# Optimization experiments

Measured on AMD Instinct MI355X. Metric: run time of the kernel, lower is better.

## Reference

```python
import jax, jax.numpy as jnp
import numpy as np

OBS, ACT, NTRAIN, BATCH = 8, 4, 128, 8
DIN = OBS + ACT


def setup_inputs() -> dict:
    key = jax.random.key(0)
    ks = jax.random.split(key, 11)
    f32 = jnp.float32
    m_x = jax.random.normal(ks[0], (BATCH, OBS), dtype=f32)
    A = 0.1 * jax.random.normal(ks[1], (BATCH, OBS, OBS), dtype=f32)
    s_x = A @ jnp.swapaxes(A, -1, -2) + 0.01 * jnp.eye(OBS, dtype=f32)  # SPD obs covariance
    m_u = jax.random.normal(ks[2], (BATCH, ACT), dtype=f32)
    Au = 0.1 * jax.random.normal(ks[3], (BATCH, ACT, ACT), dtype=f32)
    s_u = Au @ jnp.swapaxes(Au, -1, -2) + 0.01 * jnp.eye(ACT, dtype=f32)
    c_xu = 0.05 * jax.random.normal(ks[4], (BATCH, OBS, ACT), dtype=f32)
    X_train = jax.random.normal(ks[5], (NTRAIN, DIN), dtype=f32)
    lengthscales = jax.random.uniform(ks[6], (OBS, DIN), dtype=f32, minval=0.5, maxval=2.0)
    variances = jax.random.uniform(ks[7], (OBS, 1), dtype=f32, minval=0.5, maxval=1.5)
    noises = jax.random.uniform(ks[8], (OBS,), dtype=f32, minval=0.01, maxval=0.1)
    R = jax.random.normal(ks[9], (OBS, NTRAIN, NTRAIN), dtype=f32) / np.float32(np.sqrt(NTRAIN))
    inv_K = R @ jnp.swapaxes(R, -1, -2) + 0.1 * jnp.eye(NTRAIN, dtype=f32)  # SPD like a true K^-1
    beta = 0.1 * jax.random.normal(ks[10], (OBS, NTRAIN), dtype=f32)
    return dict(m_x=m_x, s_x=s_x, m_u=m_u, s_u=s_u, c_xu=c_xu, X_train=X_train,
                lengthscales=lengthscales, variances=variances, noises=noises,
                inv_K=inv_K, beta=beta)


def _forward(m_x, s_x, m_u, s_u, c_xu, X_train, lengthscales, variances, noises, inv_K, beta):
    obs_dim, input_dim = lengthscales.shape
    n = X_train.shape[0]
    eyeD = jnp.eye(input_dim, dtype=m_x.dtype)
    # joint input distribution over [x, u]
    joint_mean = jnp.concatenate([m_x, m_u], axis=-1)                      # [B, D]
    s_ = s_x @ c_xu                                                        # [B, obs, act] (as in source)
    upper = jnp.concatenate([s_x, s_], axis=-1)                            # [B, obs, D]
    lower = jnp.concatenate([jnp.swapaxes(s_, -1, -2), s_u], axis=-1)      # [B, act, D]
    joint_var = jnp.concatenate([upper, lower], axis=-2)                   # [B, D, D]
    # --- predictive mean (moment matching) ---
    inp = X_train[None, :, :] - joint_mean[:, None, :]                     # [B, N, D]
    inv_ls = 1.0 / lengthscales                                            # [E, D]
    inv_N = inp[:, None, :, :] * inv_ls[None, :, None, :]                  # [B, E, N, D]
    B_mat = inv_ls[None, :, :, None] * joint_var[:, None, :, :] * inv_ls[None, :, None, :] + eyeD
    t = jnp.swapaxes(jnp.linalg.solve(B_mat, jnp.swapaxes(inv_N, -1, -2)), -1, -2)  # [B, E, N, D]
    scaled_exp = jnp.exp(-0.5 * jnp.sum(inv_N * t, axis=-1))               # [B, E, N]
    lb = scaled_exp * beta[None, :, :]                                     # [B, E, N]
    det_B = jnp.linalg.det(B_mat)                                          # [B, E]
    var_v = variances[:, 0]                                                # [E]
    c = var_v[None, :] / jnp.sqrt(det_B)                                   # [B, E]
    pred_mean = jnp.sum(lb, axis=-1) * c                                   # [B, E]
    # --- input-output cross covariance ---
    t_inv_L = t * inv_ls[None, :, None, :]                                 # [B, E, N, D]
    cross_cov = jnp.swapaxes(jnp.einsum('bend,ben->bed', t_inv_L, lb) * c[..., None], -1, -2)  # [B, D, E]
    # --- predictive covariance: vectorized over all (a, b) output pairs ---
    X_i = X_train[:, None, :]
    X_j = X_train[None, :, :]
    diff = X_i - X_j                                                       # [N, N, D]
    l2 = lengthscales ** 2
    inv_l2 = 1.0 / l2

    def pair(l2_a, inv_a, var_a, beta_a, l2_b, inv_b, var_b, beta_b):
        inv_sum = inv_a + inv_b                                            # [D]
        Lam = 1.0 / inv_sum
        z_bar = Lam * (X_i * inv_a + X_j * inv_b)                          # [N, N, D]
        z = z_bar[None, :, :, :] - joint_mean[:, None, None, :]            # [B, N, N, D]
        z_flat = z.reshape(z.shape[0], n * n, input_dim)
        R_ab = joint_var * inv_sum[None, None, :] + eyeD                   # joint_var @ diag(inv_sum) + I
        exp1 = -0.5 * jnp.sum(diff * diff * (1.0 / (l2_a + l2_b)), axis=-1)  # [N, N]
        M_ab = joint_var + jnp.diag(Lam)[None, :, :]                       # [B, D, D]
        solved = jnp.swapaxes(jnp.linalg.solve(M_ab, jnp.swapaxes(z_flat, -1, -2)), -1, -2)
        exp2 = (-0.5 * jnp.sum(z_flat * solved, axis=-1)).reshape(z.shape[0], n, n)
        c_ab = var_a * var_b / jnp.sqrt(jnp.linalg.det(R_ab))              # [B]
        Q = c_ab[:, None, None] * jnp.exp(exp1[None, :, :] + exp2)         # [B, N, N]
        main = jnp.einsum('i,bij,j->b', beta_a, Q, beta_b)                 # [B]
        return main, Q

    pair_b = jax.vmap(pair, in_axes=(None, None, None, None, 0, 0, 0, 0))
    pair_ab = jax.vmap(pair_b, in_axes=(0, 0, 0, 0, None, None, None, None))
    main, Q = pair_ab(l2, inv_l2, var_v, beta, l2, inv_l2, var_v, beta)    # [E, E, B], [E, E, B, N, N]
    pred_cov = jnp.moveaxis(main, -1, 0)                                   # [B, E, E]
    idx = jnp.arange(obs_dim)
    Q_diag = Q[idx, idx]                                                   # [E, B, N, N]
    trace_val = jnp.einsum('eij,ebji->eb', inv_K, Q_diag)                  # [E, B]
    diag_corr = var_v[:, None] - trace_val + noises[:, None]               # [E, B]
    pred_cov = pred_cov + diag_corr.T[:, :, None] * jnp.eye(obs_dim, dtype=m_x.dtype)
    pred_cov = pred_cov - pred_mean[:, :, None] * pred_mean[:, None, :]
    pred_cov = 0.5 * (pred_cov + jnp.swapaxes(pred_cov, -1, -2))
    # --- propagate state moments ---
    cov_xf = upper @ cross_cov                                             # [B, obs, obs]
    m_out = m_x + pred_mean
    s_out = s_x + pred_cov + cov_xf + jnp.swapaxes(cov_xf, -1, -2)
    s_out = 0.5 * (s_out + jnp.swapaxes(s_out, -1, -2)) + 1e-8 * jnp.eye(obs_dim, dtype=m_x.dtype)
    return m_out, s_out


def reference(m_x, s_x, m_u, s_u, c_xu, X_train, lengthscales, variances, noises, inv_K, beta):
    return _forward(m_x, s_x, m_u, s_u, c_xu, X_train, lengthscales, variances, noises, inv_K, beta)
```

## Files before the change

### kernel.cpp

```cpp
#include <hip/hip_runtime.h>
#include <math.h>

#define OBS 8
#define ACT 4
#define DIN 12
#define NTRAIN 128
#define BATCH 8
#define NPAIR 36
#define NPT (BATCH*NPAIR)
#define NGT (BATCH*OBS)
#define NTASK (NPT+NGT)
#define HSTRIDE 68

#define WS_PM  0
#define WS_CC  64
#define WS_MN  832
#define WS_TR  1344

__global__ void __launch_bounds__(256) k_fused(
    const float* __restrict__ m_x, const float* __restrict__ s_x,
    const float* __restrict__ m_u, const float* __restrict__ s_u,
    const float* __restrict__ c_xu, const float* __restrict__ X,
    const float* __restrict__ ls, const float* __restrict__ vars,
    const float* __restrict__ beta, const float* __restrict__ invK,
    float* __restrict__ ws)
{
    int blk = blockIdx.x, tid = threadIdx.x;
    int lane = tid & 63, w = tid >> 6;
    bool isPair = blk < NPT;
    int b, a = 0, c = 0, e = 0;
    if (isPair) {
        b = blk / NPAIR;
        int rem = blk % NPAIR;
        while (rem >= OBS - a) { rem -= OBS - a; a++; }
        c = a + rem;
    } else {
        int q = blk - NPT; b = q / OBS; e = q % OBS;
    }

    __shared__ float jvs[144];
    __shared__ float Wl[144];
    __shared__ float mu[DIN];
    __shared__ float sc_wsum[DIN], sc_iA[DIN], sc_qc[DIN], sc_lam[DIN], sc_isum[DIN];
    __shared__ float s_cab;
    __shared__ __align__(16) float h[NTRAIN][HSTRIDE];
    __shared__ float red[4][13];

    int j0 = 2*lane;
    float xa[12], xb[12], xi[12];
    {
        const float4* xr = (const float4*)(X + j0*DIN);
        float4 t0 = xr[0], t1 = xr[1], t2 = xr[2], t3 = xr[3], t4 = xr[4], t5 = xr[5];
        xa[0]=t0.x; xa[1]=t0.y; xa[2]=t0.z; xa[3]=t0.w;
        xa[4]=t1.x; xa[5]=t1.y; xa[6]=t1.z; xa[7]=t1.w;
        xa[8]=t2.x; xa[9]=t2.y; xa[10]=t2.z; xa[11]=t2.w;
        xb[0]=t3.x; xb[1]=t3.y; xb[2]=t3.z; xb[3]=t3.w;
        xb[4]=t4.x; xb[5]=t4.y; xb[6]=t4.z; xb[7]=t4.w;
        xb[8]=t5.x; xb[9]=t5.y; xb[10]=t5.z; xb[11]=t5.w;
    }
    if (tid < NTRAIN) {
        const float4* xr = (const float4*)(X + tid*DIN);
        float4 t0 = xr[0], t1 = xr[1], t2 = xr[2];
        xi[0]=t0.x; xi[1]=t0.y; xi[2]=t0.z; xi[3]=t0.w;
        xi[4]=t1.x; xi[5]=t1.y; xi[6]=t1.z; xi[7]=t1.w;
        xi[8]=t2.x; xi[9]=t2.y; xi[10]=t2.z; xi[11]=t2.w;
    }

    if (tid < 144) {
        int r = tid / 12, cl = tid % 12;
        float v;
        if (r < OBS && cl < OBS) {
            v = s_x[(b*OBS+r)*OBS + cl];
        } else if (r < OBS) {
            v = 0.f;
            #pragma unroll
            for (int k = 0; k < OBS; k++)
                v += s_x[(b*OBS+r)*OBS+k] * c_xu[(b*OBS+k)*ACT + (cl-OBS)];
        } else if (cl < OBS) {
            v = 0.f;
            #pragma unroll
            for (int k = 0; k < OBS; k++)
                v += s_x[(b*OBS+cl)*OBS+k] * c_xu[(b*OBS+k)*ACT + (r-OBS)];
        } else {
            v = s_u[(b*ACT+r-OBS)*ACT + (cl-OBS)];
        }
        jvs[tid] = v;
    } else if (tid >= 160 && tid < 172) {
        int d = tid - 160;
        mu[d] = (d < OBS) ? m_x[b*OBS+d] : m_u[b*ACT+d-OBS];
    } else if (tid >= 192 && tid < 204) {
        int d = tid - 192;
        if (isPair) {
            float la = ls[a*DIN+d]; la *= la;
            float lc = ls[c*DIN+d]; lc *= lc;
            float ia = 1.f/la, ic = 1.f/lc;
            float is = ia + ic;
            float L  = 1.f/is;
            sc_wsum[d] = 1.f/(la+lc);
            sc_iA[d] = L*ia;
            sc_qc[d] = L*ic;
            sc_lam[d] = L;
            sc_isum[d] = is;
        } else {
            sc_iA[d] = 1.f / ls[e*DIN+d];
        }
    }
    __syncthreads();

    if (tid < DIN) {
        int r = tid;
        float row[12];
        if (isPair) {
            #pragma unroll
            for (int j = 0; j < 12; j++) row[j] = jvs[r*12+j];
            row[r] += sc_lam[r];
        } else {
            float ir = sc_iA[r];
            #pragma unroll
            for (int j = 0; j < 12; j++) row[j] = ir * sc_iA[j] * jvs[r*12+j];
            row[r] += 1.f;
        }
        float det = 1.f;
        #pragma unroll
        for (int k = 0; k < 12; k++) {
            float p = __shfl(row[k], k);
            float ip = 1.f / p;
            det *= p;
            float prow[12];
            #pragma unroll
            for (int j = 0; j < 12; j++) prow[j] = __shfl(row[j], k) * ip;
            if (r == k) {
                #pragma unroll
                for (int j = 0; j < 12; j++) row[j] = prow[j];
                row[k] = ip;
            } else {
                float f = row[k];
                #pragma unroll
                for (int j = 0; j < 12; j++) if (j != k) row[j] -= f * prow[j];
                row[k] = -f * ip;
            }
        }
        #pragma unroll
        for (int j = 0; j < 12; j++) Wl[r*12+j] = row[j];
        if (r == 0) {
            if (isPair) {
                float s = det;
                #pragma unroll
                for (int d = 0; d < 12; d++) s *= sc_isum[d];
                s_cab = vars[a]*vars[c] / sqrtf(s);
            } else {
                s_cab = vars[e] / sqrtf(det);
            }
        }
    }
    __syncthreads();

    if (isPair) {
        bool diag = (a == c);
        if (tid < NTRAIN) {
            int i = tid;
            float r[12]; float e1 = 0.f;
            #pragma unroll
            for (int d = 0; d < 12; d++) {
                r[d] = sc_iA[d]*xi[d] - mu[d];
                e1 += sc_wsum[d]*xi[d]*xi[d];
            }
            float hrow[16];
            float alpha = 0.f;
            #pragma unroll
            for (int d = 0; d < 12; d++) {
                float u = 0.f;
                #pragma unroll
                for (int cl = 0; cl < 12; cl++) u += Wl[d*12+cl]*r[cl];
                alpha += r[d]*u;
                hrow[d] = sc_wsum[d]*xi[d] - u*sc_qc[d];
            }
            hrow[12] = -0.5f*(e1 + alpha);
            hrow[13] = beta[a*NTRAIN+i];
            hrow[14] = 0.f; hrow[15] = 0.f;
            float4* hp = (float4*)&h[i][0];
            hp[0] = make_float4(hrow[0],hrow[1],hrow[2],hrow[3]);
            hp[1] = make_float4(hrow[4],hrow[5],hrow[6],hrow[7]);
            hp[2] = make_float4(hrow[8],hrow[9],hrow[10],hrow[11]);
            hp[3] = make_float4(hrow[12],hrow[13],hrow[14],hrow[15]);
        }
        float basej0, basej1, wc0, wc1;
        {
            float q0[12], q1[12]; float e10 = 0.f, e11 = 0.f;
            #pragma unroll
            for (int d = 0; d < 12; d++) {
                q0[d] = sc_qc[d]*xa[d];
                q1[d] = sc_qc[d]*xb[d];
                e10 += sc_wsum[d]*xa[d]*xa[d];
                e11 += sc_wsum[d]*xb[d]*xb[d];
            }
            float bq0 = 0.f, bq1 = 0.f;
            #pragma unroll
            for (int d = 0; d < 12; d++) {
                float u0 = 0.f, u1 = 0.f;
                #pragma unroll
                for (int cl = 0; cl < 12; cl++) {
                    float wv = Wl[d*12+cl];
                    u0 += wv*q0[cl];
                    u1 += wv*q1[cl];
                }
                bq0 += q0[d]*u0;
                bq1 += q1[d]*u1;
            }
            basej0 = -0.5f*(e10 + bq0);
            basej1 = -0.5f*(e11 + bq1);
            wc0 = beta[c*NTRAIN + j0];
            wc1 = beta[c*NTRAIN + j0 + 1];
        }
        __syncthreads();
        float am0 = 0.f, am1 = 0.f, at0 = 0.f, at1 = 0.f;
        const float2* Kb = (const float2*)(invK + a*NTRAIN*NTRAIN);
        #pragma unroll 4
        for (int k = 0; k < 32; k++) {
            int i = w + 4*k;
            const float4* hp = (const float4*)&h[i][0];
            float4 h0 = hp[0], h1 = hp[1], h2 = hp[2], h3 = hp[3];
            float sA0 = fmaf(h0.x,xa[0], fmaf(h0.y,xa[1], fmaf(h0.z,xa[2], h0.w*xa[3])));
            float sB0 = fmaf(h1.x,xa[4], fmaf(h1.y,xa[5], fmaf(h1.z,xa[6], h1.w*xa[7])));
            float sC0 = fmaf(h2.x,xa[8], fmaf(h2.y,xa[9], fmaf(h2.z,xa[10], h2.w*xa[11])));
            float sA1 = fmaf(h0.x,xb[0], fmaf(h0.y,xb[1], fmaf(h0.z,xb[2], h0.w*xb[3])));
            float sB1 = fmaf(h1.x,xb[4], fmaf(h1.y,xb[5], fmaf(h1.z,xb[6], h1.w*xb[7])));
            float sC1 = fmaf(h2.x,xb[8], fmaf(h2.y,xb[9], fmaf(h2.z,xb[10], h2.w*xb[11])));
            float e0 = __expf(sA0 + sB0 + sC0 + h3.x + basej0);
            float e1v = __expf(sA1 + sB1 + sC1 + h3.x + basej1);
            am0 = fmaf(h3.y, e0, am0);
            am1 = fmaf(h3.y, e1v, am1);
            if (diag) {
                float2 kv = Kb[i*64 + lane];
                at0 = fmaf(kv.x, e0, at0);
                at1 = fmaf(kv.y, e1v, at1);
            }
        }
        float accm = am0*wc0 + am1*wc1;
        float acct = at0 + at1;
        #pragma unroll
        for (int off = 32; off >= 1; off >>= 1) {
            accm += __shfl_xor(accm, off, 64);
            acct += __shfl_xor(acct, off, 64);
        }
        if (lane == 0) { red[w][0] = accm; red[w][1] = acct; }
        __syncthreads();
        if (tid == 0) {
            float m = (red[0][0]+red[1][0]+red[2][0]+red[3][0]) * s_cab;
            ws[WS_MN + b*64 + a*8 + c] = m;
            ws[WS_MN + b*64 + c*8 + a] = m;
            if (diag)
                ws[WS_TR + b*8 + a] = (red[0][1]+red[1][1]+red[2][1]+red[3][1]) * s_cab;
        }
    } else {
        float vals[13];
        #pragma unroll
        for (int v = 0; v < 13; v++) vals[v] = 0.f;
        if (tid < NTRAIN) {
            int n = tid;
            float iN[12];
            #pragma unroll
            for (int d = 0; d < 12; d++) iN[d] = (xi[d]-mu[d]) * sc_iA[d];
            float qq = 0.f; float tv[12];
            #pragma unroll
            for (int d = 0; d < 12; d++) {
                float u = 0.f;
                #pragma unroll
                for (int cl = 0; cl < 12; cl++) u += Wl[d*12+cl]*iN[cl];
                tv[d] = u; qq += iN[d]*u;
            }
            float lb = __expf(-0.5f*qq) * beta[e*NTRAIN+n];
            vals[0] = lb;
            #pragma unroll
            for (int d = 0; d < 12; d++) vals[1+d] = tv[d]*sc_iA[d]*lb;
        }
        #pragma unroll
        for (int v = 0; v < 13; v++)
            #pragma unroll
            for (int off = 32; off >= 1; off >>= 1) vals[v] += __shfl_xor(vals[v], off, 64);
        if (lane == 0) {
            #pragma unroll
            for (int v = 0; v < 13; v++) red[w][v] = vals[v];
        }
        __syncthreads();
        if (tid == 0) {
            float cn = s_cab;
            ws[WS_PM + b*OBS + e] = cn*(red[0][0]+red[1][0]);
            for (int d = 0; d < 12; d++)
                ws[WS_CC + (b*DIN+d)*OBS + e] = cn*(red[0][1+d]+red[1][1+d]);
        }
    }
}

__global__ void k_final(const float* __restrict__ m_x, const float* __restrict__ s_x,
                        const float* __restrict__ c_xu, const float* __restrict__ vars,
                        const float* __restrict__ noises, const float* __restrict__ ws,
                        float* __restrict__ out) {
    int b = blockIdx.x, t = threadIdx.x;
    __shared__ float pm[OBS];
    __shared__ float sxs[64];
    const float* cc = ws + WS_CC + b*DIN*OBS;
    const float* mn = ws + WS_MN + b*64;
    const float* tr = ws + WS_TR + b*OBS;
    sxs[t] = s_x[b*64 + t];
    if (t < OBS) {
        float p = ws[WS_PM + b*OBS + t];
        pm[t] = p;
        out[b*OBS + t] = m_x[b*OBS + t] + p;
    }
    __syncthreads();
    int r = t >> 3, cl = t & 7;
    float P = mn[r*8 + cl];
    if (r == cl) P += vars[r] - tr[r] + noises[r];
    P -= pm[r]*pm[cl];
    float cxf = 0.f, cxfT = 0.f;
    #pragma unroll
    for (int d = 0; d < 8; d++) {
        cxf  += sxs[r*8+d]  * cc[d*8+cl];
        cxfT += sxs[cl*8+d] * cc[d*8+r];
    }
    #pragma unroll
    for (int d = 0; d < 4; d++) {
        float jr = 0.f, jc = 0.f;
        #pragma unroll
        for (int k = 0; k < 8; k++) {
            float cx = c_xu[(b*OBS+k)*ACT + d];
            jr += sxs[r*8+k]  * cx;
            jc += sxs[cl*8+k] * cx;
        }
        cxf  += jr * cc[(8+d)*8 + cl];
        cxfT += jc * cc[(8+d)*8 + r];
    }
    float S = sxs[r*8+cl] + P + cxf + cxfT;
    if (r == cl) S += 1e-8f;
    out[64 + b*64 + t] = S;
}

extern "C" void kernel_launch(void* const* d_in, const int* in_sizes, int n_in,
                              void* d_out, int out_size, void* d_ws, size_t ws_size,
                              hipStream_t stream) {
    const float* m_x    = (const float*)d_in[0];
    const float* s_x    = (const float*)d_in[1];
    const float* m_u    = (const float*)d_in[2];
    const float* s_u    = (const float*)d_in[3];
    const float* c_xu   = (const float*)d_in[4];
    const float* X      = (const float*)d_in[5];
    const float* ls     = (const float*)d_in[6];
    const float* vars   = (const float*)d_in[7];
    const float* noises = (const float*)d_in[8];
    const float* invK   = (const float*)d_in[9];
    const float* beta   = (const float*)d_in[10];
    float* out = (float*)d_out;
    float* ws  = (float*)d_ws;

    k_fused<<<NTASK, 256, 0, stream>>>(m_x, s_x, m_u, s_u, c_xu, X, ls, vars,
                                       beta, invK, ws);
    k_final<<<BATCH, 64, 0, stream>>>(m_x, s_x, c_xu, vars, noises, ws, out);
}
```

Before: 92.27 us.

## Double block size, precompute per-point bases in shared memory, shrink h stride

```diff
diff --git a/kernel.cpp b/kernel.cpp
--- a/kernel.cpp
+++ b/kernel.cpp
@@ -10,14 +10,15 @@
 #define NPT (BATCH*NPAIR)
 #define NGT (BATCH*OBS)
 #define NTASK (NPT+NGT)
-#define HSTRIDE 68
+#define THREADS 512
+#define HSTRIDE 16
 
 #define WS_PM  0
 #define WS_CC  64
 #define WS_MN  832
 #define WS_TR  1344
 
-__global__ void __launch_bounds__(256) k_fused(
+__global__ void __launch_bounds__(THREADS) k_fused(
     const float* __restrict__ m_x, const float* __restrict__ s_x,
     const float* __restrict__ m_u, const float* __restrict__ s_u,
     const float* __restrict__ c_xu, const float* __restrict__ X,
@@ -44,7 +45,8 @@
     __shared__ float sc_wsum[DIN], sc_iA[DIN], sc_qc[DIN], sc_lam[DIN], sc_isum[DIN];
     __shared__ float s_cab;
     __shared__ __align__(16) float h[NTRAIN][HSTRIDE];
-    __shared__ float red[4][13];
+    __shared__ __align__(16) float2 bw[NTRAIN];
+    __shared__ float red[8][13];
 
     int j0 = 2*lane;
     float xa[12], xb[12], xi[12];
@@ -158,75 +160,57 @@
     if (isPair) {
         bool diag = (a == c);
         if (tid < NTRAIN) {
-            int i = tid;
-            float r[12]; float e1 = 0.f;
+            int t = tid;
+            float r[12], q[12]; float e1 = 0.f;
             #pragma unroll
             for (int d = 0; d < 12; d++) {
                 r[d] = sc_iA[d]*xi[d] - mu[d];
+                q[d] = sc_qc[d]*xi[d];
                 e1 += sc_wsum[d]*xi[d]*xi[d];
             }
             float hrow[16];
-            float alpha = 0.f;
+            float alpha = 0.f, bq = 0.f;
             #pragma unroll
             for (int d = 0; d < 12; d++) {
-                float u = 0.f;
-                #pragma unroll
-                for (int cl = 0; cl < 12; cl++) u += Wl[d*12+cl]*r[cl];
+                float u = 0.f, uq = 0.f;
+                #pragma unroll
+                for (int cl = 0; cl < 12; cl++) {
+                    float wv = Wl[d*12+cl];
+                    u  += wv*r[cl];
+                    uq += wv*q[cl];
+                }
                 alpha += r[d]*u;
+                bq    += q[d]*uq;
                 hrow[d] = sc_wsum[d]*xi[d] - u*sc_qc[d];
             }
             hrow[12] = -0.5f*(e1 + alpha);
-            hrow[13] = beta[a*NTRAIN+i];
+            hrow[13] = beta[a*NTRAIN+t];
             hrow[14] = 0.f; hrow[15] = 0.f;
-            float4* hp = (float4*)&h[i][0];
+            float4* hp = (float4*)&h[t][0];
             hp[0] = make_float4(hrow[0],hrow[1],hrow[2],hrow[3]);
             hp[1] = make_float4(hrow[4],hrow[5],hrow[6],hrow[7]);
             hp[2] = make_float4(hrow[8],hrow[9],hrow[10],hrow[11]);
             hp[3] = make_float4(hrow[12],hrow[13],hrow[14],hrow[15]);
-        }
-        float basej0, basej1, wc0, wc1;
-        {
-            float q0[12], q1[12]; float e10 = 0.f, e11 = 0.f;
-            #pragma unroll
-            for (int d = 0; d < 12; d++) {
-                q0[d] = sc_qc[d]*xa[d];
-                q1[d] = sc_qc[d]*xb[d];
-                e10 += sc_wsum[d]*xa[d]*xa[d];
-                e11 += sc_wsum[d]*xb[d]*xb[d];
-            }
-            float bq0 = 0.f, bq1 = 0.f;
-            #pragma unroll
-            for (int d = 0; d < 12; d++) {
-                float u0 = 0.f, u1 = 0.f;
-                #pragma unroll
-                for (int cl = 0; cl < 12; cl++) {
-                    float wv = Wl[d*12+cl];
-                    u0 += wv*q0[cl];
-                    u1 += wv*q1[cl];
-                }
-                bq0 += q0[d]*u0;
-                bq1 += q1[d]*u1;
-            }
-            basej0 = -0.5f*(e10 + bq0);
-            basej1 = -0.5f*(e11 + bq1);
-            wc0 = beta[c*NTRAIN + j0];
-            wc1 = beta[c*NTRAIN + j0 + 1];
+            bw[t] = make_float2(-0.5f*(e1 + bq), beta[c*NTRAIN+t]);
         }
         __syncthreads();
+        float4 bwv = ((const float4*)bw)[lane];
+        float basej0 = bwv.x, wc0 = bwv.y, basej1 = bwv.z, wc1 = bwv.w;
         float am0 = 0.f, am1 = 0.f, at0 = 0.f, at1 = 0.f;
         const float2* Kb = (const float2*)(invK + a*NTRAIN*NTRAIN);
         #pragma unroll 4
-        for (int k = 0; k < 32; k++) {
-            int i = w + 4*k;
+        for (int k = 0; k < 16; k++) {
+            int i = w + 8*k;
             const float4* hp = (const float4*)&h[i][0];
-            float4 h0 = hp[0], h1 = hp[1], h2 = hp[2], h3 = hp[3];
+            float4 h0 = hp[0], h1 = hp[1], h2 = hp[2];
+            float2 h3 = *(const float2*)&h[i][12];
             float sA0 = fmaf(h0.x,xa[0], fmaf(h0.y,xa[1], fmaf(h0.z,xa[2], h0.w*xa[3])));
             float sB0 = fmaf(h1.x,xa[4], fmaf(h1.y,xa[5], fmaf(h1.z,xa[6], h1.w*xa[7])));
             float sC0 = fmaf(h2.x,xa[8], fmaf(h2.y,xa[9], fmaf(h2.z,xa[10], h2.w*xa[11])));
             float sA1 = fmaf(h0.x,xb[0], fmaf(h0.y,xb[1], fmaf(h0.z,xb[2], h0.w*xb[3])));
             float sB1 = fmaf(h1.x,xb[4], fmaf(h1.y,xb[5], fmaf(h1.z,xb[6], h1.w*xb[7])));
             float sC1 = fmaf(h2.x,xb[8], fmaf(h2.y,xb[9], fmaf(h2.z,xb[10], h2.w*xb[11])));
-            float e0 = __expf(sA0 + sB0 + sC0 + h3.x + basej0);
+            float e0  = __expf(sA0 + sB0 + sC0 + h3.x + basej0);
             float e1v = __expf(sA1 + sB1 + sC1 + h3.x + basej1);
             am0 = fmaf(h3.y, e0, am0);
             am1 = fmaf(h3.y, e1v, am1);
@@ -246,11 +230,13 @@
         if (lane == 0) { red[w][0] = accm; red[w][1] = acct; }
         __syncthreads();
         if (tid == 0) {
-            float m = (red[0][0]+red[1][0]+red[2][0]+red[3][0]) * s_cab;
+            float m = 0.f, t = 0.f;
+            #pragma unroll
+            for (int v = 0; v < 8; v++) { m += red[v][0]; t += red[v][1]; }
+            m *= s_cab; t *= s_cab;
             ws[WS_MN + b*64 + a*8 + c] = m;
             ws[WS_MN + b*64 + c*8 + a] = m;
-            if (diag)
-                ws[WS_TR + b*8 + a] = (red[0][1]+red[1][1]+red[2][1]+red[3][1]) * s_cab;
+            if (diag) ws[WS_TR + b*8 + a] = t;
         }
     } else {
         float vals[13];
@@ -353,7 +339,7 @@
     float* out = (float*)d_out;
     float* ws  = (float*)d_ws;
 
-    k_fused<<<NTASK, 256, 0, stream>>>(m_x, s_x, m_u, s_u, c_xu, X, ls, vars,
-                                       beta, invK, ws);
+    k_fused<<<NTASK, THREADS, 0, stream>>>(m_x, s_x, m_u, s_u, c_xu, X, ls, vars,
+                                           beta, invK, ws);
     k_final<<<BATCH, 64, 0, stream>>>(m_x, s_x, c_xu, vars, noises, ws, out);
 }
```

Result: no change. 91.46 us (-0.9%).
